# Performance work log

Hardware: AMD Instinct MI355X
Metric: run time of the kernel (lower is better)

The kernel has to match this reference:

```python
import jax, jax.numpy as jnp
import numpy as np

N = 50000
E = 800000
IN_CH, HID, OUT_CH = 8, 64, 1
NEG_SLOPE = 0.2


def setup_inputs() -> dict:
    key = jax.random.key(0)
    ks = jax.random.split(key, 16)
    x = jax.random.normal(ks[0], (N, IN_CH), dtype=jnp.float32)
    edge_index = jax.random.randint(ks[1], (2, E), 0, N, dtype=jnp.int64)
    def glorot(k, shape):
        fan = shape[0] + shape[-1]
        return jax.random.uniform(k, shape, jnp.float32, -1.0, 1.0) * jnp.sqrt(6.0 / fan)
    # layer 1: in=8 -> 4 heads x 64, concat=False (mean over heads)
    W1 = glorot(ks[2], (IN_CH, 4 * HID))
    as1 = glorot(ks[3], (4, HID)); ad1 = glorot(ks[4], (4, HID))
    b1 = jnp.zeros((HID,), jnp.float32)
    # layer 2: 64 -> 4 heads x 64
    W2 = glorot(ks[5], (HID, 4 * HID))
    as2 = glorot(ks[6], (4, HID)); ad2 = glorot(ks[7], (4, HID))
    b2 = jnp.zeros((HID,), jnp.float32)
    # layer 3: 64 -> 1 head x 1
    W3 = glorot(ks[8], (HID, OUT_CH))
    as3 = glorot(ks[9], (1, OUT_CH)); ad3 = glorot(ks[10], (1, OUT_CH))
    b3 = jnp.zeros((OUT_CH,), jnp.float32)
    return {"x": x, "edge_index": edge_index,
            "W1": W1, "b1": b1, "as1": as1, "ad1": ad1,
            "W2": W2, "b2": b2, "as2": as2, "ad2": ad2,
            "W3": W3, "b3": b3, "as3": as3, "ad3": ad3}


def gat_conv(x, src, dst, W, b, a_src, a_dst, n_nodes):
    """PyG GATConv, concat=False (mean over heads), add_self_loops already applied."""
    heads, ch = a_src.shape
    h = (x @ W).reshape(n_nodes, heads, ch)            # [N,H,C]
    e_src = jnp.sum(h * a_src[None], axis=-1)          # [N,H]
    e_dst = jnp.sum(h * a_dst[None], axis=-1)          # [N,H]
    logits = jax.nn.leaky_relu(e_src[src] + e_dst[dst], NEG_SLOPE)  # [E,H]
    # softmax over incoming edges of each destination node (self loops ensure non-empty)
    m = jax.ops.segment_max(logits, dst, num_segments=n_nodes)      # [N,H]
    ex = jnp.exp(logits - m[dst])
    denom = jax.ops.segment_sum(ex, dst, num_segments=n_nodes)      # [N,H]
    alpha = ex / (denom[dst] + 1e-16)                  # [E,H]
    out = jax.ops.segment_sum(alpha[:, :, None] * h[src], dst, num_segments=n_nodes)  # [N,H,C]
    return jnp.mean(out, axis=1) + b                   # [N,C]


def reference(x, edge_index, W1, b1, as1, ad1, W2, b2, as2, ad2, W3, b3, as3, ad3):
    n = x.shape[0]
    loops = jnp.arange(n, dtype=edge_index.dtype)
    src = jnp.concatenate([edge_index[0], loops])
    dst = jnp.concatenate([edge_index[1], loops])
    h = jax.nn.elu(gat_conv(x, src, dst, W1, b1, as1, ad1, n))
    # Dropout(p=0.2) is identity in eval mode
    h = jax.nn.elu(gat_conv(h, src, dst, W2, b2, as2, ad2, n))
    out = jax.nn.sigmoid(gat_conv(h, src, dst, W3, b3, as3, ad3, n))
    return out  # [N,1] failure probability per node
```

## Files before the change

kernel.cpp:

```cpp
#include <hip/hip_runtime.h>
#include <hip/hip_bf16.h>
#include <hip/hip_fp16.h>
#include <math.h>

#define N_NODES 50000
#define N_EDGES 800000
#define N_TOT   (N_EDGES + N_NODES)
#define NEG_SLOPE 0.2f

static __device__ __forceinline__ float lrelu(float x){ return x >= 0.f ? x : NEG_SLOPE * x; }

__global__ void k_detect(const int* __restrict__ ei, int* __restrict__ flag){
  if (blockIdx.x == 0 && threadIdx.x == 0){
    int o = 0;
    #pragma unroll
    for (int i = 1; i < 16; i += 2) o |= ei[i];
    *flag = (o == 0) ? 1 : 0;
  }
}

__global__ void k_init(int* __restrict__ deg, int* __restrict__ fill){
  int i = blockIdx.x * blockDim.x + threadIdx.x;
  if (i < N_NODES){ deg[i] = 1; fill[i] = 0; }
}

__global__ void k_count(const int* __restrict__ ei, const int* __restrict__ flag,
                        int* __restrict__ deg){
  int e = blockIdx.x * blockDim.x + threadIdx.x;
  if (e >= N_EDGES) return;
  int f = *flag;
  int d = f ? ei[2*(N_EDGES + e)] : ei[N_EDGES + e];
  atomicAdd(&deg[d], 1);
}

__global__ void k_scan1(const int* __restrict__ deg, int* __restrict__ rowptr,
                        int* __restrict__ bsum){
  __shared__ int sd[256];
  int t = threadIdx.x;
  int base = blockIdx.x * 1024 + t * 4;
  int v0 = (base + 0 < N_NODES) ? deg[base + 0] : 0;
  int v1 = (base + 1 < N_NODES) ? deg[base + 1] : 0;
  int v2 = (base + 2 < N_NODES) ? deg[base + 2] : 0;
  int v3 = (base + 3 < N_NODES) ? deg[base + 3] : 0;
  int tsum = v0 + v1 + v2 + v3;
  sd[t] = tsum; __syncthreads();
  for (int off = 1; off < 256; off <<= 1){
    int vv = (t >= off) ? sd[t - off] : 0;
    __syncthreads();
    sd[t] += vv;
    __syncthreads();
  }
  int excl = sd[t] - tsum;
  if (base + 0 < N_NODES) rowptr[base + 0] = excl;
  if (base + 1 < N_NODES) rowptr[base + 1] = excl + v0;
  if (base + 2 < N_NODES) rowptr[base + 2] = excl + v0 + v1;
  if (base + 3 < N_NODES) rowptr[base + 3] = excl + v0 + v1 + v2;
  if (t == 255) bsum[blockIdx.x] = sd[255];
}

#define NB_SCAN 49
__global__ void k_scan2(const int* __restrict__ bsum, int* __restrict__ boff){
  int t = threadIdx.x;
  int v = (t < NB_SCAN) ? bsum[t] : 0;
  int incl = v;
  #pragma unroll
  for (int off = 1; off < 64; off <<= 1){
    int u = __shfl_up(incl, off);
    if (t >= off) incl += u;
  }
  if (t < NB_SCAN) boff[t] = incl - v;
}

__global__ void k_scan3(int* __restrict__ rowptr, const int* __restrict__ boff){
  int i = blockIdx.x * blockDim.x + threadIdx.x;
  if (i < N_NODES) rowptr[i] += boff[i >> 10];
  if (i == 0) rowptr[N_NODES] = N_TOT;
}

__global__ void k_scatter(const int* __restrict__ ei, const int* __restrict__ flag,
                          const int* __restrict__ rowptr, int* __restrict__ fill,
                          int* __restrict__ col){
  int e = blockIdx.x * blockDim.x + threadIdx.x;
  if (e >= N_TOT) return;
  int s, d;
  if (e < N_EDGES){
    int f = *flag;
    if (f){ s = ei[2*e]; d = ei[2*(N_EDGES + e)]; }
    else  { s = ei[e];   d = ei[N_EDGES + e]; }
  } else {
    s = d = e - N_EDGES;
  }
  int pos = atomicAdd(&fill[d], 1);
  col[rowptr[d] + pos] = s;
}


__global__ __launch_bounds__(256) void k_transform1(
    const float* __restrict__ xin, const float* __restrict__ W,
    const float* __restrict__ aS, const float* __restrict__ aD,
    __half* __restrict__ h, float* __restrict__ es, float* __restrict__ ed){
  __shared__ float wl[8 * 256];
  int tid = threadIdx.x;
  for (int i = tid; i < 8 * 256; i += 256) wl[i] = W[i];
  int lane = tid & 63, wv = tid >> 6, head = lane >> 4;
  float4 s4 = *(const float4*)&aS[4 * lane];
  float4 d4 = *(const float4*)&aD[4 * lane];
  __syncthreads();
  int base = (blockIdx.x * 4 + wv) * 8;
  for (int m = 0; m < 8; m++){
    int n = base + m;
    if (n >= N_NODES) break;
    float4 xa = *(const float4*)&xin[n * 8];
    float4 xb = *(const float4*)&xin[n * 8 + 4];
    float xs0 = xa.x, xs1 = xa.y, xs2 = xa.z, xs3 = xa.w;
    float xs4 = xb.x, xs5 = xb.y, xs6 = xb.z, xs7 = xb.w;
    float4 acc = make_float4(0.f, 0.f, 0.f, 0.f);
    #define T1STEP(k, xv) { float4 w4 = *(const float4*)&wl[(k)*256 + 4*lane]; \
      acc.x = fmaf(xv, w4.x, acc.x); acc.y = fmaf(xv, w4.y, acc.y); \
      acc.z = fmaf(xv, w4.z, acc.z); acc.w = fmaf(xv, w4.w, acc.w); }
    T1STEP(0, xs0) T1STEP(1, xs1) T1STEP(2, xs2) T1STEP(3, xs3)
    T1STEP(4, xs4) T1STEP(5, xs5) T1STEP(6, xs6) T1STEP(7, xs7)
    #undef T1STEP
    __half2 p0 = __floats2half2_rn(acc.x, acc.y);
    __half2 p1 = __floats2half2_rn(acc.z, acc.w);
    uint2 u; u.x = *(unsigned int*)&p0; u.y = *(unsigned int*)&p1;
    *(uint2*)&h[(size_t)n * 256 + 4 * lane] = u;
    float ps = acc.x*s4.x + acc.y*s4.y + acc.z*s4.z + acc.w*s4.w;
    float pd = acc.x*d4.x + acc.y*d4.y + acc.z*d4.z + acc.w*d4.w;
    #pragma unroll
    for (int off = 1; off < 16; off <<= 1){ ps += __shfl_xor(ps, off); pd += __shfl_xor(pd, off); }
    if ((lane & 15) == 0){ es[n * 4 + head] = ps; ed[n * 4 + head] = pd; }
  }
}

__global__ __launch_bounds__(256) void k_transform2(
    const float* __restrict__ xin, const float* __restrict__ W,
    const float* __restrict__ aS, const float* __restrict__ aD,
    __half* __restrict__ h, float* __restrict__ es, float* __restrict__ ed){
  __shared__ float wl[32 * 256];
  int tid = threadIdx.x;
  int lane = tid & 63, wv = tid >> 6, head = lane >> 4;
  float4 s4 = *(const float4*)&aS[4 * lane];
  float4 d4 = *(const float4*)&aD[4 * lane];
  int base = (blockIdx.x * 4 + wv) * 8;
  float xr[8];
  #pragma unroll
  for (int m = 0; m < 8; m++){
    int n = base + m;
    xr[m] = (n < N_NODES) ? xin[(size_t)n * 64 + lane] : 0.f;
  }
  float4 acc[8];
  #pragma unroll
  for (int m = 0; m < 8; m++) acc[m] = make_float4(0.f, 0.f, 0.f, 0.f);
  for (int hf = 0; hf < 2; hf++){
    if (hf) __syncthreads();
    const float4* Wv = (const float4*)(W + hf * 32 * 256);
    float4* wlv = (float4*)wl;
    #pragma unroll
    for (int i = 0; i < 8; i++) wlv[tid + 256 * i] = Wv[tid + 256 * i];
    __syncthreads();
    #pragma unroll 4
    for (int k = 0; k < 32; k++){
      float4 w4 = *(const float4*)&wl[k * 256 + 4 * lane];
      #pragma unroll
      for (int m = 0; m < 8; m++){
        float xv = __shfl(xr[m], hf * 32 + k);
        acc[m].x = fmaf(xv, w4.x, acc[m].x);
        acc[m].y = fmaf(xv, w4.y, acc[m].y);
        acc[m].z = fmaf(xv, w4.z, acc[m].z);
        acc[m].w = fmaf(xv, w4.w, acc[m].w);
      }
    }
  }
  #pragma unroll
  for (int m = 0; m < 8; m++){
    int n = base + m;
    if (n >= N_NODES) break;
    __half2 p0 = __floats2half2_rn(acc[m].x, acc[m].y);
    __half2 p1 = __floats2half2_rn(acc[m].z, acc[m].w);
    uint2 u; u.x = *(unsigned int*)&p0; u.y = *(unsigned int*)&p1;
    *(uint2*)&h[(size_t)n * 256 + 4 * lane] = u;
    float ps = acc[m].x*s4.x + acc[m].y*s4.y + acc[m].z*s4.z + acc[m].w*s4.w;
    float pd = acc[m].x*d4.x + acc[m].y*d4.y + acc[m].z*d4.z + acc[m].w*d4.w;
    #pragma unroll
    for (int off = 1; off < 16; off <<= 1){ ps += __shfl_xor(ps, off); pd += __shfl_xor(pd, off); }
    if ((lane & 15) == 0){ es[n * 4 + head] = ps; ed[n * 4 + head] = pd; }
  }
}

__global__ __launch_bounds__(256) void k_transform3(
    const float* __restrict__ xin, const float* __restrict__ W3,
    const float* __restrict__ aS, const float* __restrict__ aD,
    float* __restrict__ h3, float* __restrict__ es3, float* __restrict__ ed3){
  int gid = blockIdx.x * blockDim.x + threadIdx.x;
  int n = gid >> 6, lane = gid & 63;
  if (n >= N_NODES) return;
  float v = xin[(size_t)n * 64 + lane] * W3[lane];
  #pragma unroll
  for (int off = 1; off < 64; off <<= 1) v += __shfl_xor(v, off);
  if (lane == 0){
    h3[n] = v;
    es3[n] = v * aS[0];
    ed3[n] = v * aD[0];
  }
}

__global__ __launch_bounds__(256) void k_agg(
    const __half* __restrict__ h, const float* __restrict__ es, const float* __restrict__ ed,
    const int* __restrict__ rowptr, const int* __restrict__ col,
    const float* __restrict__ bias, float* __restrict__ outf){
  int gid = blockIdx.x * blockDim.x + threadIdx.x;
  int d = gid >> 6, lane = gid & 63;
  if (d >= N_NODES) return;
  int start = rowptr[d], end = rowptr[d + 1];
  int head = lane >> 4;
  float eh = ed[d * 4 + head];
  const __half* hp = h + 4 * lane;
  float4 acc = make_float4(0.f, 0.f, 0.f, 0.f);
  float wsum = 0.f;
  int i = start;
  for (; i + 4 <= end; i += 4){
    int s0 = col[i], s1 = col[i + 1], s2 = col[i + 2], s3 = col[i + 3];
    uint2 u0 = *(const uint2*)(hp + (size_t)s0 * 256);
    uint2 u1 = *(const uint2*)(hp + (size_t)s1 * 256);
    uint2 u2 = *(const uint2*)(hp + (size_t)s2 * 256);
    uint2 u3 = *(const uint2*)(hp + (size_t)s3 * 256);
    float e0 = es[s0 * 4 + head], e1 = es[s1 * 4 + head];
    float e2 = es[s2 * 4 + head], e3 = es[s3 * 4 + head];
    float w0 = __expf(lrelu(e0 + eh));
    float w1 = __expf(lrelu(e1 + eh));
    float w2 = __expf(lrelu(e2 + eh));
    float w3 = __expf(lrelu(e3 + eh));
    wsum += (w0 + w1) + (w2 + w3);
    float2 a0 = __half22float2(*(__half2*)&u0.x), b0 = __half22float2(*(__half2*)&u0.y);
    float2 a1 = __half22float2(*(__half2*)&u1.x), b1 = __half22float2(*(__half2*)&u1.y);
    float2 a2 = __half22float2(*(__half2*)&u2.x), b2 = __half22float2(*(__half2*)&u2.y);
    float2 a3 = __half22float2(*(__half2*)&u3.x), b3 = __half22float2(*(__half2*)&u3.y);
    acc.x = fmaf(w0, a0.x, acc.x); acc.y = fmaf(w0, a0.y, acc.y);
    acc.z = fmaf(w0, b0.x, acc.z); acc.w = fmaf(w0, b0.y, acc.w);
    acc.x = fmaf(w1, a1.x, acc.x); acc.y = fmaf(w1, a1.y, acc.y);
    acc.z = fmaf(w1, b1.x, acc.z); acc.w = fmaf(w1, b1.y, acc.w);
    acc.x = fmaf(w2, a2.x, acc.x); acc.y = fmaf(w2, a2.y, acc.y);
    acc.z = fmaf(w2, b2.x, acc.z); acc.w = fmaf(w2, b2.y, acc.w);
    acc.x = fmaf(w3, a3.x, acc.x); acc.y = fmaf(w3, a3.y, acc.y);
    acc.z = fmaf(w3, b3.x, acc.z); acc.w = fmaf(w3, b3.y, acc.w);
  }
  for (; i < end; i++){
    int s0 = col[i];
    uint2 u0 = *(const uint2*)(hp + (size_t)s0 * 256);
    float w0 = __expf(lrelu(es[s0 * 4 + head] + eh));
    wsum += w0;
    float2 a0 = __half22float2(*(__half2*)&u0.x), b0 = __half22float2(*(__half2*)&u0.y);
    acc.x = fmaf(w0, a0.x, acc.x); acc.y = fmaf(w0, a0.y, acc.y);
    acc.z = fmaf(w0, b0.x, acc.z); acc.w = fmaf(w0, b0.y, acc.w);
  }
  float inv = 1.0f / (wsum + 1e-16f);
  acc.x *= inv; acc.y *= inv; acc.z *= inv; acc.w *= inv;
  #pragma unroll
  for (int off = 16; off < 64; off <<= 1){
    acc.x += __shfl_xor(acc.x, off);
    acc.y += __shfl_xor(acc.y, off);
    acc.z += __shfl_xor(acc.z, off);
    acc.w += __shfl_xor(acc.w, off);
  }
  if (lane < 16){
    float4 b4 = *(const float4*)&bias[4 * lane];
    float ox = 0.25f * acc.x + b4.x;
    float oy = 0.25f * acc.y + b4.y;
    float oz = 0.25f * acc.z + b4.z;
    float ow = 0.25f * acc.w + b4.w;
    ox = ox > 0.f ? ox : expm1f(ox);
    oy = oy > 0.f ? oy : expm1f(oy);
    oz = oz > 0.f ? oz : expm1f(oz);
    ow = ow > 0.f ? ow : expm1f(ow);
    float4 o = make_float4(ox, oy, oz, ow);
    *(float4*)&outf[(size_t)d * 64 + 4 * lane] = o;
  }
}

__global__ __launch_bounds__(256) void k_agg3(
    const float* __restrict__ h3, const float* __restrict__ es3, const float* __restrict__ ed3,
    const int* __restrict__ rowptr, const int* __restrict__ col,
    const float* __restrict__ b3, float* __restrict__ out){
  int gid = blockIdx.x * blockDim.x + threadIdx.x;
  int wv = gid >> 6, lane = gid & 63;
  int sub = lane >> 4, li = lane & 15;
  int d = wv * 4 + sub;
  if (d < N_NODES){
    int start = rowptr[d], end = rowptr[d + 1];
    float edv = ed3[d];
    float num = 0.f, den = 0.f;
    for (int i = start + li; i < end; i += 16){
      int s = col[i];
      float wgt = __expf(lrelu(es3[s] + edv));
      den += wgt;
      num = fmaf(wgt, h3[s], num);
    }
    #pragma unroll
    for (int off = 1; off < 16; off <<= 1){
      num += __shfl_xor(num, off);
      den += __shfl_xor(den, off);
    }
    if (li == 0){
      float v = num / (den + 1e-16f) + b3[0];
      out[d] = 1.f / (1.f + __expf(-v));
    }
  }
}

extern "C" void kernel_launch(void* const* d_in, const int* in_sizes, int n_in,
                              void* d_out, int out_size, void* d_ws, size_t ws_size,
                              hipStream_t stream) {
  const float* x   = (const float*)d_in[0];
  const int*   ei  = (const int*)  d_in[1];
  const float* W1  = (const float*)d_in[2];
  const float* b1  = (const float*)d_in[3];
  const float* as1 = (const float*)d_in[4];
  const float* ad1 = (const float*)d_in[5];
  const float* W2  = (const float*)d_in[6];
  const float* b2  = (const float*)d_in[7];
  const float* as2 = (const float*)d_in[8];
  const float* ad2 = (const float*)d_in[9];
  const float* W3  = (const float*)d_in[10];
  const float* b3  = (const float*)d_in[11];
  const float* as3 = (const float*)d_in[12];
  const float* ad3 = (const float*)d_in[13];
  float* out = (float*)d_out;

  char* w = (char*)d_ws;
  size_t off = 0;
  auto alloc = [&](size_t bytes) -> char* {
    char* p = w + off;
    off += (bytes + 255) & ~size_t(255);
    return p;
  };
  int*    flag   = (int*)   alloc(64);
  int*    deg    = (int*)   alloc(N_NODES * 4);
  int*    fill   = (int*)   alloc(N_NODES * 4);
  int*    rowptr = (int*)   alloc((N_NODES + 1) * 4);
  int*    bsum   = (int*)   alloc(64 * 4);
  int*    boff   = (int*)   alloc(64 * 4);
  int*    col    = (int*)   alloc((size_t)N_TOT * 4);
  __half* h      = (__half*)alloc((size_t)N_NODES * 256 * 2);
  float*  es     = (float*) alloc((size_t)N_NODES * 4 * 4);
  float*  ed     = (float*) alloc((size_t)N_NODES * 4 * 4);
  float*  feat1  = (float*) alloc((size_t)N_NODES * 64 * 4);
  float*  feat2  = (float*) alloc((size_t)N_NODES * 64 * 4);
  float*  h3     = (float*) alloc(N_NODES * 4);
  float*  es3    = (float*) alloc(N_NODES * 4);
  float*  ed3    = (float*) alloc(N_NODES * 4);
  (void)ws_size; (void)in_sizes; (void)n_in; (void)out_size;

  k_detect <<<1, 64, 0, stream>>>(ei, flag);
  k_init   <<<(N_NODES + 255) / 256, 256, 0, stream>>>(deg, fill);
  k_count  <<<(N_EDGES + 255) / 256, 256, 0, stream>>>(ei, flag, deg);
  k_scan1  <<<NB_SCAN, 256, 0, stream>>>(deg, rowptr, bsum);
  k_scan2  <<<1, 64, 0, stream>>>(bsum, boff);
  k_scan3  <<<(N_NODES + 255) / 256, 256, 0, stream>>>(rowptr, boff);
  k_scatter<<<(N_TOT + 255) / 256, 256, 0, stream>>>(ei, flag, rowptr, fill, col);

  const int grid_t12 = (N_NODES + 31) / 32;
  const int grid_wpn = (N_NODES * 64 + 255) / 256;
  const int grid_w4n = ((N_NODES + 3) / 4 * 64 + 255) / 256;

  k_transform1<<<grid_t12, 256, 0, stream>>>(x, W1, as1, ad1, h, es, ed);
  k_agg       <<<grid_wpn, 256, 0, stream>>>(h, es, ed, rowptr, col, b1, feat1);
  k_transform2<<<grid_t12, 256, 0, stream>>>(feat1, W2, as2, ad2, h, es, ed);
  k_agg       <<<grid_wpn, 256, 0, stream>>>(h, es, ed, rowptr, col, b2, feat2);
  k_transform3<<<grid_wpn, 256, 0, stream>>>(feat2, W3, as3, ad3, h3, es3, ed3);
  k_agg3      <<<grid_w4n, 256, 0, stream>>>(h3, es3, ed3, rowptr, col, b3, out);
}
```

Baseline: 392.8 us.

## Streamline CSR build, widen edge loads, unroll aggregation and pack layer-3 data

Several changes are bundled together. The detect kernel is merged into init. Count and scatter now handle two edges per thread with vector loads. The scatter fill counter is seeded with rowptr, which removes a lookup. The aggregation loop gathers 8 neighbours per iteration instead of 4, and transform2's inner loop is fully unrolled. Layer-3 es and h are packed into a float2 so each edge does one gather. These cut launch count, memory transactions and gather latency, at the cost of higher register pressure in the unrolled loops.

```diff
diff --git a/kernel.cpp b/kernel.cpp
--- a/kernel.cpp
+++ b/kernel.cpp
@@ -10,27 +10,32 @@
 
 static __device__ __forceinline__ float lrelu(float x){ return x >= 0.f ? x : NEG_SLOPE * x; }
 
-__global__ void k_detect(const int* __restrict__ ei, int* __restrict__ flag){
-  if (blockIdx.x == 0 && threadIdx.x == 0){
+__global__ void k_init(const int* __restrict__ ei, int* __restrict__ flag,
+                       int* __restrict__ deg){
+  int i = blockIdx.x * blockDim.x + threadIdx.x;
+  if (i == 0){
     int o = 0;
     #pragma unroll
-    for (int i = 1; i < 16; i += 2) o |= ei[i];
+    for (int j = 1; j < 16; j += 2) o |= ei[j];
     *flag = (o == 0) ? 1 : 0;
   }
-}
-
-__global__ void k_init(int* __restrict__ deg, int* __restrict__ fill){
-  int i = blockIdx.x * blockDim.x + threadIdx.x;
-  if (i < N_NODES){ deg[i] = 1; fill[i] = 0; }
+  if (i < N_NODES) deg[i] = 1;
 }
 
 __global__ void k_count(const int* __restrict__ ei, const int* __restrict__ flag,
                         int* __restrict__ deg){
-  int e = blockIdx.x * blockDim.x + threadIdx.x;
-  if (e >= N_EDGES) return;
-  int f = *flag;
-  int d = f ? ei[2*(N_EDGES + e)] : ei[N_EDGES + e];
-  atomicAdd(&deg[d], 1);
+  int t = blockIdx.x * blockDim.x + threadIdx.x;
+  if (t >= N_EDGES / 2) return;
+  int d0, d1;
+  if (*flag){
+    int4 dv = *(const int4*)&ei[2 * N_EDGES + 4 * t];
+    d0 = dv.x; d1 = dv.z;
+  } else {
+    int2 dv = *(const int2*)&ei[N_EDGES + 2 * t];
+    d0 = dv.x; d1 = dv.y;
+  }
+  atomicAdd(&deg[d0], 1);
+  atomicAdd(&deg[d1], 1);
 }
 
 __global__ void k_scan1(const int* __restrict__ deg, int* __restrict__ rowptr,
@@ -71,27 +76,37 @@
   if (t < NB_SCAN) boff[t] = incl - v;
 }
 
-__global__ void k_scan3(int* __restrict__ rowptr, const int* __restrict__ boff){
+__global__ void k_scan3(int* __restrict__ rowptr, const int* __restrict__ boff,
+                        int* __restrict__ fill){
   int i = blockIdx.x * blockDim.x + threadIdx.x;
-  if (i < N_NODES) rowptr[i] += boff[i >> 10];
+  if (i < N_NODES){
+    int v = rowptr[i] + boff[i >> 10];
+    rowptr[i] = v;
+    fill[i] = v;
+  }
   if (i == 0) rowptr[N_NODES] = N_TOT;
 }
 
 __global__ void k_scatter(const int* __restrict__ ei, const int* __restrict__ flag,
-                          const int* __restrict__ rowptr, int* __restrict__ fill,
-                          int* __restrict__ col){
-  int e = blockIdx.x * blockDim.x + threadIdx.x;
-  if (e >= N_TOT) return;
-  int s, d;
-  if (e < N_EDGES){
-    int f = *flag;
-    if (f){ s = ei[2*e]; d = ei[2*(N_EDGES + e)]; }
-    else  { s = ei[e];   d = ei[N_EDGES + e]; }
+                          int* __restrict__ fill, int* __restrict__ col){
+  int t = blockIdx.x * blockDim.x + threadIdx.x;
+  if (t < N_EDGES / 2){
+    int s0, s1, d0, d1;
+    if (*flag){
+      int4 sv = *(const int4*)&ei[4 * t];
+      int4 dv = *(const int4*)&ei[2 * N_EDGES + 4 * t];
+      s0 = sv.x; s1 = sv.z; d0 = dv.x; d1 = dv.z;
+    } else {
+      int2 sv = *(const int2*)&ei[2 * t];
+      int2 dv = *(const int2*)&ei[N_EDGES + 2 * t];
+      s0 = sv.x; s1 = sv.y; d0 = dv.x; d1 = dv.y;
+    }
+    col[atomicAdd(&fill[d0], 1)] = s0;
+    col[atomicAdd(&fill[d1], 1)] = s1;
   } else {
-    s = d = e - N_EDGES;
-  }
-  int pos = atomicAdd(&fill[d], 1);
-  col[rowptr[d] + pos] = s;
+    int n = t - N_EDGES / 2;
+    if (n < N_NODES) col[atomicAdd(&fill[n], 1)] = n;
+  }
 }
 
 
@@ -152,6 +167,7 @@
   float4 acc[8];
   #pragma unroll
   for (int m = 0; m < 8; m++) acc[m] = make_float4(0.f, 0.f, 0.f, 0.f);
+  #pragma unroll
   for (int hf = 0; hf < 2; hf++){
     if (hf) __syncthreads();
     const float4* Wv = (const float4*)(W + hf * 32 * 256);
@@ -159,7 +175,7 @@
     #pragma unroll
     for (int i = 0; i < 8; i++) wlv[tid + 256 * i] = Wv[tid + 256 * i];
     __syncthreads();
-    #pragma unroll 4
+    #pragma unroll
     for (int k = 0; k < 32; k++){
       float4 w4 = *(const float4*)&wl[k * 256 + 4 * lane];
       #pragma unroll
@@ -191,7 +207,7 @@
 __global__ __launch_bounds__(256) void k_transform3(
     const float* __restrict__ xin, const float* __restrict__ W3,
     const float* __restrict__ aS, const float* __restrict__ aD,
-    float* __restrict__ h3, float* __restrict__ es3, float* __restrict__ ed3){
+    float2* __restrict__ pk, float* __restrict__ ed3){
   int gid = blockIdx.x * blockDim.x + threadIdx.x;
   int n = gid >> 6, lane = gid & 63;
   if (n >= N_NODES) return;
@@ -199,10 +215,16 @@
   #pragma unroll
   for (int off = 1; off < 64; off <<= 1) v += __shfl_xor(v, off);
   if (lane == 0){
-    h3[n] = v;
-    es3[n] = v * aS[0];
+    pk[n] = make_float2(v * aS[0], v);
     ed3[n] = v * aD[0];
   }
+}
+
+static __device__ __forceinline__ void agg_step(float4& acc, uint2 u, float wt){
+  float2 aa = __half22float2(*(__half2*)&u.x);
+  float2 bb = __half22float2(*(__half2*)&u.y);
+  acc.x = fmaf(wt, aa.x, acc.x); acc.y = fmaf(wt, aa.y, acc.y);
+  acc.z = fmaf(wt, bb.x, acc.z); acc.w = fmaf(wt, bb.y, acc.w);
 }
 
 __global__ __launch_bounds__(256) void k_agg(
@@ -219,40 +241,37 @@
   float4 acc = make_float4(0.f, 0.f, 0.f, 0.f);
   float wsum = 0.f;
   int i = start;
-  for (; i + 4 <= end; i += 4){
-    int s0 = col[i], s1 = col[i + 1], s2 = col[i + 2], s3 = col[i + 3];
+  for (; i + 8 <= end; i += 8){
+    int s0 = col[i],     s1 = col[i + 1], s2 = col[i + 2], s3 = col[i + 3];
+    int s4 = col[i + 4], s5 = col[i + 5], s6 = col[i + 6], s7 = col[i + 7];
     uint2 u0 = *(const uint2*)(hp + (size_t)s0 * 256);
     uint2 u1 = *(const uint2*)(hp + (size_t)s1 * 256);
     uint2 u2 = *(const uint2*)(hp + (size_t)s2 * 256);
     uint2 u3 = *(const uint2*)(hp + (size_t)s3 * 256);
+    uint2 u4 = *(const uint2*)(hp + (size_t)s4 * 256);
+    uint2 u5 = *(const uint2*)(hp + (size_t)s5 * 256);
+    uint2 u6 = *(const uint2*)(hp + (size_t)s6 * 256);
+    uint2 u7 = *(const uint2*)(hp + (size_t)s7 * 256);
     float e0 = es[s0 * 4 + head], e1 = es[s1 * 4 + head];
     float e2 = es[s2 * 4 + head], e3 = es[s3 * 4 + head];
-    float w0 = __expf(lrelu(e0 + eh));
-    float w1 = __expf(lrelu(e1 + eh));
-    float w2 = __expf(lrelu(e2 + eh));
-    float w3 = __expf(lrelu(e3 + eh));
-    wsum += (w0 + w1) + (w2 + w3);
-    float2 a0 = __half22float2(*(__half2*)&u0.x), b0 = __half22float2(*(__half2*)&u0.y);
-    float2 a1 = __half22float2(*(__half2*)&u1.x), b1 = __half22float2(*(__half2*)&u1.y);
-    float2 a2 = __half22float2(*(__half2*)&u2.x), b2 = __half22float2(*(__half2*)&u2.y);
-    float2 a3 = __half22float2(*(__half2*)&u3.x), b3 = __half22float2(*(__half2*)&u3.y);
-    acc.x = fmaf(w0, a0.x, acc.x); acc.y = fmaf(w0, a0.y, acc.y);
-    acc.z = fmaf(w0, b0.x, acc.z); acc.w = fmaf(w0, b0.y, acc.w);
-    acc.x = fmaf(w1, a1.x, acc.x); acc.y = fmaf(w1, a1.y, acc.y);
-    acc.z = fmaf(w1, b1.x, acc.z); acc.w = fmaf(w1, b1.y, acc.w);
-    acc.x = fmaf(w2, a2.x, acc.x); acc.y = fmaf(w2, a2.y, acc.y);
-    acc.z = fmaf(w2, b2.x, acc.z); acc.w = fmaf(w2, b2.y, acc.w);
-    acc.x = fmaf(w3, a3.x, acc.x); acc.y = fmaf(w3, a3.y, acc.y);
-    acc.z = fmaf(w3, b3.x, acc.z); acc.w = fmaf(w3, b3.y, acc.w);
+    float e4 = es[s4 * 4 + head], e5 = es[s5 * 4 + head];
+    float e6 = es[s6 * 4 + head], e7 = es[s7 * 4 + head];
+    float w0 = __expf(lrelu(e0 + eh)), w1 = __expf(lrelu(e1 + eh));
+    float w2 = __expf(lrelu(e2 + eh)), w3 = __expf(lrelu(e3 + eh));
+    float w4 = __expf(lrelu(e4 + eh)), w5 = __expf(lrelu(e5 + eh));
+    float w6 = __expf(lrelu(e6 + eh)), w7 = __expf(lrelu(e7 + eh));
+    wsum += ((w0 + w1) + (w2 + w3)) + ((w4 + w5) + (w6 + w7));
+    agg_step(acc, u0, w0); agg_step(acc, u1, w1);
+    agg_step(acc, u2, w2); agg_step(acc, u3, w3);
+    agg_step(acc, u4, w4); agg_step(acc, u5, w5);
+    agg_step(acc, u6, w6); agg_step(acc, u7, w7);
   }
   for (; i < end; i++){
     int s0 = col[i];
     uint2 u0 = *(const uint2*)(hp + (size_t)s0 * 256);
     float w0 = __expf(lrelu(es[s0 * 4 + head] + eh));
     wsum += w0;
-    float2 a0 = __half22float2(*(__half2*)&u0.x), b0 = __half22float2(*(__half2*)&u0.y);
-    acc.x = fmaf(w0, a0.x, acc.x); acc.y = fmaf(w0, a0.y, acc.y);
-    acc.z = fmaf(w0, b0.x, acc.z); acc.w = fmaf(w0, b0.y, acc.w);
+    agg_step(acc, u0, w0);
   }
   float inv = 1.0f / (wsum + 1e-16f);
   acc.x *= inv; acc.y *= inv; acc.z *= inv; acc.w *= inv;
@@ -279,7 +298,7 @@
 }
 
 __global__ __launch_bounds__(256) void k_agg3(
-    const float* __restrict__ h3, const float* __restrict__ es3, const float* __restrict__ ed3,
+    const float2* __restrict__ pk, const float* __restrict__ ed3,
     const int* __restrict__ rowptr, const int* __restrict__ col,
     const float* __restrict__ b3, float* __restrict__ out){
   int gid = blockIdx.x * blockDim.x + threadIdx.x;
@@ -291,10 +310,10 @@
     float edv = ed3[d];
     float num = 0.f, den = 0.f;
     for (int i = start + li; i < end; i += 16){
-      int s = col[i];
-      float wgt = __expf(lrelu(es3[s] + edv));
+      float2 p = pk[col[i]];
+      float wgt = __expf(lrelu(p.x + edv));
       den += wgt;
-      num = fmaf(wgt, h3[s], num);
+      num = fmaf(wgt, p.y, num);
     }
     #pragma unroll
     for (int off = 1; off < 16; off <<= 1){
@@ -346,18 +365,16 @@
   float*  ed     = (float*) alloc((size_t)N_NODES * 4 * 4);
   float*  feat1  = (float*) alloc((size_t)N_NODES * 64 * 4);
   float*  feat2  = (float*) alloc((size_t)N_NODES * 64 * 4);
-  float*  h3     = (float*) alloc(N_NODES * 4);
-  float*  es3    = (float*) alloc(N_NODES * 4);
+  float2* pk     = (float2*)alloc((size_t)N_NODES * 8);
   float*  ed3    = (float*) alloc(N_NODES * 4);
   (void)ws_size; (void)in_sizes; (void)n_in; (void)out_size;
 
-  k_detect <<<1, 64, 0, stream>>>(ei, flag);
-  k_init   <<<(N_NODES + 255) / 256, 256, 0, stream>>>(deg, fill);
-  k_count  <<<(N_EDGES + 255) / 256, 256, 0, stream>>>(ei, flag, deg);
+  k_init   <<<(N_NODES + 255) / 256, 256, 0, stream>>>(ei, flag, deg);
+  k_count  <<<(N_EDGES / 2 + 255) / 256, 256, 0, stream>>>(ei, flag, deg);
   k_scan1  <<<NB_SCAN, 256, 0, stream>>>(deg, rowptr, bsum);
   k_scan2  <<<1, 64, 0, stream>>>(bsum, boff);
-  k_scan3  <<<(N_NODES + 255) / 256, 256, 0, stream>>>(rowptr, boff);
-  k_scatter<<<(N_TOT + 255) / 256, 256, 0, stream>>>(ei, flag, rowptr, fill, col);
+  k_scan3  <<<(N_NODES + 255) / 256, 256, 0, stream>>>(rowptr, boff, fill);
+  k_scatter<<<(N_EDGES / 2 + N_NODES + 255) / 256, 256, 0, stream>>>(ei, flag, fill, col);
 
   const int grid_t12 = (N_NODES + 31) / 32;
   const int grid_wpn = (N_NODES * 64 + 255) / 256;
@@ -367,6 +384,6 @@
   k_agg       <<<grid_wpn, 256, 0, stream>>>(h, es, ed, rowptr, col, b1, feat1);
   k_transform2<<<grid_t12, 256, 0, stream>>>(feat1, W2, as2, ad2, h, es, ed);
   k_agg       <<<grid_wpn, 256, 0, stream>>>(h, es, ed, rowptr, col, b2, feat2);
-  k_transform3<<<grid_wpn, 256, 0, stream>>>(feat2, W3, as3, ad3, h3, es3, ed3);
-  k_agg3      <<<grid_w4n, 256, 0, stream>>>(h3, es3, ed3, rowptr, col, b3, out);
-}
+  k_transform3<<<grid_wpn, 256, 0, stream>>>(feat2, W3, as3, ad3, pk, ed3);
+  k_agg3      <<<grid_w4n, 256, 0, stream>>>(pk, ed3, rowptr, col, b3, out);
+}
```

New measurement: 1.261 ms. 221% more time.
